# Performance work log

Measured on AMD Instinct MI355X. Metric: run time of the kernel, lower is better.

## Reference

```python
import jax, jax.numpy as jnp
import numpy as np

TEMPERATURE = 30.0
NUM_KERNELS = 4


def setup_inputs() -> dict:
    key = jax.random.key(0)
    ks = jax.random.split(key, 7)
    B, H, W, C = 32, 56, 56, 256
    F, KH, KW, K = 256, 3, 3, NUM_KERNELS
    hidden = C // 4  # attention_reduction_ratio = 4
    x = jax.random.normal(ks[0], (B, H, W, C), dtype=jnp.float32)
    # K parallel conv kernels (HWIO layout) and biases
    fan = KH * KW * C
    kernels = jax.random.normal(ks[1], (K, KH, KW, C, F), dtype=jnp.float32) / np.sqrt(fan)
    biases = jnp.zeros((K, F), dtype=jnp.float32)
    # attention MLP: GAP -> Dense(C//4, relu) -> Dense(K)
    w1 = jax.random.normal(ks[2], (C, hidden), dtype=jnp.float32) / np.sqrt(C)
    b1 = jnp.zeros((hidden,), dtype=jnp.float32)
    w2 = jax.random.normal(ks[3], (hidden, K), dtype=jnp.float32) / np.sqrt(hidden)
    b2 = jnp.zeros((K,), dtype=jnp.float32)
    return {"x": x, "kernels": kernels, "biases": biases,
            "w1": w1, "b1": b1, "w2": w2, "b2": b2}


def reference(x, kernels, biases, w1, b1, w2, b2):
    # Attention router: GAP -> Dense(relu) -> Dense(K) -> softmax(logits / tau)
    pooled = jnp.mean(x, axis=(1, 2))                       # [B, C]
    h = jax.nn.relu(pooled @ w1 + b1)                       # [B, C//4]
    logits = h @ w2 + b2                                    # [B, K]
    attn = jax.nn.softmax(logits / TEMPERATURE, axis=-1)    # [B, K]

    # K parallel conv branches (stride 1, SAME padding, dilation 1, groups 1)
    def conv_k(w, b):
        y = jax.lax.conv_general_dilated(
            x, w, window_strides=(1, 1), padding='SAME',
            dimension_numbers=('NHWC', 'HWIO', 'NHWC'))
        return y + b                                        # [B, H, W, F]

    ys = jax.vmap(conv_k)(kernels, biases)                  # [K, B, H, W, F]
    # per-sample weighted aggregation of branch outputs
    out = jnp.einsum('kbhwf,bk->bhwf', ys, attn)            # [B, H, W, F]
    return out
```

## Files before the change

kernel.cpp:

```cpp
#include <hip/hip_runtime.h>
#include <hip/hip_bf16.h>
#include <stdint.h>

typedef __bf16 bf16_t;
typedef __bf16 bf16x4 __attribute__((ext_vector_type(4)));
typedef __bf16 bf16x8 __attribute__((ext_vector_type(8)));
typedef float floatx4 __attribute__((ext_vector_type(4)));

#define B_ 32
#define HP 58
#define WP 66

#define XPAD_OFF   0u
#define WAGG_OFF   62717952u
#define POOLED_OFF 100466688u
#define ATTN_OFF   100499456u
#define BIASAGG_OFF 100499968u

__device__ __forceinline__ void async_copy16(const void* gsrc, void* ldst) {
  __builtin_amdgcn_global_load_lds(
      (const __attribute__((address_space(1))) unsigned int*)gsrc,
      (__attribute__((address_space(3))) unsigned int*)ldst, 16, 0, 0);
}

__global__ __launch_bounds__(256)
void pad_pool(const float* __restrict__ x, bf16_t* __restrict__ xpad,
              float* __restrict__ pooled) {
  const int hp = blockIdx.x;
  const int b  = blockIdx.y;
  const int t  = threadIdx.x;
  const int c4 = (t & 63) << 2;
  const int wq = t >> 6;
  const int h  = hp - 1;
  const bool hvalid = (h >= 0) && (h < 56);
  bf16_t* dst = xpad + ((size_t)(b * 58 + hp)) * (66 * 256);
  const float* srcrow = x + ((size_t)(b * 56 + (hvalid ? h : 0))) * (56 * 256);
  floatx4 sum = {0.f, 0.f, 0.f, 0.f};
  for (int wp = wq; wp < 66; wp += 4) {
    const int w = wp - 1;
    floatx4 v = {0.f, 0.f, 0.f, 0.f};
    if (hvalid && (unsigned)w < 56u) {
      v = *(const floatx4*)(srcrow + w * 256 + c4);
      sum += v;
    }
    bf16x4 r;
#pragma unroll
    for (int j = 0; j < 4; ++j) r[j] = (bf16_t)v[j];
    *(bf16x4*)(dst + wp * 256 + c4) = r;
  }
  __shared__ floatx4 red[4][64];
  red[wq][t & 63] = sum;
  __syncthreads();
  if (hvalid && t < 64) {
    floatx4 s = red[0][t] + red[1][t] + red[2][t] + red[3][t];
#pragma unroll
    for (int j = 0; j < 4; ++j) atomicAdd(&pooled[b * 256 + t * 4 + j], s[j]);
  }
}

__global__ __launch_bounds__(256)
void router(const float* __restrict__ pooled, const float* __restrict__ w1,
            const float* __restrict__ b1, const float* __restrict__ w2,
            const float* __restrict__ b2, const float* __restrict__ biases,
            float* __restrict__ attn, float* __restrict__ biasagg) {
  __shared__ float ps[8192];
  __shared__ float w1s[16384];
  __shared__ float hs[2048];
  __shared__ float lg[128];
  __shared__ float at[128];
  const int t = threadIdx.x;
  for (int i = t; i < 8192; i += 256) ps[i] = pooled[i] * (1.0f / 3136.0f);
  for (int i = t; i < 4096; i += 256)
    *(floatx4*)&w1s[i * 4] = *(const floatx4*)&w1[i * 4];
  __syncthreads();
  for (int task = t; task < 2048; task += 256) {
    const int b = task >> 6, j = task & 63;
    const float* pb = ps + b * 256;
    float s0 = 0.f, s1 = 0.f, s2 = 0.f, s3 = 0.f;
#pragma unroll 4
    for (int c = 0; c < 256; c += 4) {
      s0 += pb[c]     * w1s[c * 64 + j];
      s1 += pb[c + 1] * w1s[(c + 1) * 64 + j];
      s2 += pb[c + 2] * w1s[(c + 2) * 64 + j];
      s3 += pb[c + 3] * w1s[(c + 3) * 64 + j];
    }
    hs[task] = fmaxf((s0 + s1) + (s2 + s3) + b1[j], 0.f);
  }
  __syncthreads();
  if (t < 128) {
    int b = t >> 2, k = t & 3;
    float s = b2[k];
    const float* hb = hs + b * 64;
#pragma unroll 4
    for (int j = 0; j < 64; ++j) s += hb[j] * w2[j * 4 + k];
    lg[t] = s * (1.0f / 30.0f);
  }
  __syncthreads();
  if (t < 32) {
    int b = t;
    float z0 = lg[b*4], z1 = lg[b*4+1], z2 = lg[b*4+2], z3 = lg[b*4+3];
    float m = fmaxf(fmaxf(z0, z1), fmaxf(z2, z3));
    float e0 = expf(z0-m), e1 = expf(z1-m), e2 = expf(z2-m), e3 = expf(z3-m);
    float inv = 1.0f / (e0 + e1 + e2 + e3);
    at[b*4] = e0*inv; at[b*4+1] = e1*inv; at[b*4+2] = e2*inv; at[b*4+3] = e3*inv;
    attn[b*4] = at[b*4]; attn[b*4+1] = at[b*4+1];
    attn[b*4+2] = at[b*4+2]; attn[b*4+3] = at[b*4+3];
  }
  __syncthreads();
  for (int i = t; i < 8192; i += 256) {
    int b = i >> 8, f = i & 255;
    biasagg[i] = at[b*4]*biases[f] + at[b*4+1]*biases[256+f]
               + at[b*4+2]*biases[512+f] + at[b*4+3]*biases[768+f];
  }
}

__global__ __launch_bounds__(256)
void wagg_kernel(const float* __restrict__ kers, const float* __restrict__ attn,
                 bf16_t* __restrict__ wagg) {
  const int lid = blockIdx.x;
  const int xcd = lid & 7;
  const int sl  = lid >> 3;
  const int c8  = sl & 7;
  const int tap = sl >> 3;
  const int b0  = xcd << 2;
  const int t   = threadIdx.x;
  __shared__ bf16_t tile[4][32 * 260];

  float a[4][4];
#pragma unroll
  for (int i = 0; i < 4; ++i)
#pragma unroll
    for (int k = 0; k < 4; ++k) a[i][k] = attn[(b0 + i) * 4 + k];

  const float* k0 = kers + ((size_t)(0 * 9 + tap)) * 65536 + (size_t)(c8 * 32) * 256;
  const float* k1 = kers + ((size_t)(1 * 9 + tap)) * 65536 + (size_t)(c8 * 32) * 256;
  const float* k2 = kers + ((size_t)(2 * 9 + tap)) * 65536 + (size_t)(c8 * 32) * 256;
  const float* k3 = kers + ((size_t)(3 * 9 + tap)) * 65536 + (size_t)(c8 * 32) * 256;

  const int fq = t & 63;
  const int cl = t >> 6;
  const int f0 = fq * 4;
#pragma unroll
  for (int pass = 0; pass < 8; ++pass) {
    const int c_local = pass * 4 + cl;
    const size_t o = (size_t)c_local * 256 + f0;
    floatx4 v0 = *(const floatx4*)(k0 + o);
    floatx4 v1 = *(const floatx4*)(k1 + o);
    floatx4 v2 = *(const floatx4*)(k2 + o);
    floatx4 v3 = *(const floatx4*)(k3 + o);
#pragma unroll
    for (int i = 0; i < 4; ++i) {
      bf16x4 r;
#pragma unroll
      for (int j = 0; j < 4; ++j)
        r[j] = (bf16_t)(a[i][0] * v0[j] + a[i][1] * v1[j] + a[i][2] * v2[j] + a[i][3] * v3[j]);
      *(bf16x4*)&tile[i][c_local * 260 + f0] = r;
    }
  }
  __syncthreads();

#pragma unroll
  for (int i = 0; i < 4; ++i) {
    bf16_t* wt = wagg + ((size_t)((b0 + i) * 9 + tap)) * 65536 + c8 * 32;
#pragma unroll
    for (int pass = 0; pass < 4; ++pass) {
      const int gi = pass * 256 + t;
      const int f  = gi >> 2;
      const int cg = gi & 3;
      bf16x8 v;
#pragma unroll
      for (int jj = 0; jj < 8; ++jj) v[jj] = tile[i][(cg * 8 + jj) * 260 + f];
      *(bf16x8*)(wt + (size_t)f * 256 + cg * 8) = v;
    }
  }
}

#define PBUF_BYTES 40960

__global__ __launch_bounds__(512, 2)
void conv_mfma(const bf16_t* __restrict__ xpad, const bf16_t* __restrict__ wagg,
               const float* __restrict__ biasagg, float* __restrict__ out) {
  __shared__ char lds[2 * PBUF_BYTES];
  char* ldsP0 = lds;
  char* ldsP1 = lds + PBUF_BYTES;

  const int lid  = blockIdx.y * 14 + blockIdx.x;
  const int nid  = (lid & 7) * 56 + (lid >> 3);
  const int b    = nid / 14;
  const int tile = nid - b * 14;
  const int h0 = (tile >> 1) * 8;
  const int w0 = (tile & 1) * 28;

  const int tid  = threadIdx.x;
  const int lane = tid & 63;
  const int wv   = tid >> 6;
  const int mg   = wv >> 2;
  const int fs   = wv & 3;
  const int l15  = lane & 15;
  const int quad = lane >> 4;
  const int n0   = fs * 64;

  const char* xb = (const char*)xpad + (size_t)b * (HP * WP * 256 * 2);
  const char* wb = (const char*)wagg + (size_t)b * (9 * 256 * 256 * 2);

  int offs[7];
#pragma unroll
  for (int mi = 0; mi < 7; ++mi) {
    int m = mg * 112 + mi * 16 + l15;
    int ty = m / 28;
    int tx = m - ty * 28;
    offs[mi] = ty * 32 + tx;
  }
  const char* bbase = wb + (size_t)(n0 + l15) * 512 + quad * 16;
  int sp_off[5];
#pragma unroll
  for (int ii = 0; ii < 5; ++ii) {
    int i40 = wv * 5 + ii;
    int p = i40 * 8 + (lane >> 3);
    int row = p >> 5, col = p & 31;
    int gsrc = (lane & 7) ^ (p & 7);
    sp_off[ii] = ((h0 + row) * WP + (w0 + col)) * 512 + gsrc * 16;
  }

  floatx4 acc[7][4];
#pragma unroll
  for (int mi = 0; mi < 7; ++mi)
#pragma unroll
    for (int ni = 0; ni < 4; ++ni) acc[mi][ni] = (floatx4){0.f, 0.f, 0.f, 0.f};

  auto stage_patch = [&](int cq, char* pdst) {
#pragma unroll
    for (int ii = 0; ii < 5; ++ii)
      async_copy16(xb + cq * 128 + sp_off[ii], pdst + (wv * 5 + ii) * 1024);
  };
  auto load_B = [&](int cq, int tap, bf16x8* dst) {
    const char* base = bbase + (size_t)tap * 131072 + cq * 128;
#pragma unroll
    for (int ni = 0; ni < 4; ++ni) {
      dst[ni]     = *(const bf16x8*)(base + ni * 8192);
      dst[4 + ni] = *(const bf16x8*)(base + ni * 8192 + 64);
    }
  };

  stage_patch(0, ldsP0);
  asm volatile("s_waitcnt vmcnt(0)" ::: "memory");
  __builtin_amdgcn_s_barrier();
  __builtin_amdgcn_sched_barrier(0);

  bf16x8 Bcur[8], Bnext[8];
  load_B(0, 0, Bcur);

  bf16x8 aA[7], aB[7];

#pragma unroll 1
  for (int d = 0; d < 36; ++d) {
    const int cq  = d / 9;
    const int tap = d - cq * 9;
    char* pbc = (cq & 1) ? ldsP1 : ldsP0;
    char* pbn = (cq & 1) ? ldsP0 : ldsP1;
    const bool haveNext = (d < 35);

    if (tap == 0 && cq < 3) stage_patch(cq + 1, pbn);

    if (haveNext) {
      const int nt = (tap == 8) ? 0 : tap + 1;
      const int nc = (tap == 8) ? cq + 1 : cq;
      load_B(nc, nt, Bnext);
    }

    const int tapoff = (tap / 3) * 32 + (tap % 3);
    int aoff[7];
#pragma unroll
    for (int mi = 0; mi < 7; ++mi) {
      int p = offs[mi] + tapoff;
      aoff[mi] = (p << 7) + ((quad ^ (p & 7)) << 4);
      aA[mi] = *(const bf16x8*)(pbc + aoff[mi]);
    }

    __builtin_amdgcn_s_setprio(1);
#pragma unroll
    for (int mi = 0; mi < 7; ++mi) {
      acc[mi][0] = __builtin_amdgcn_mfma_f32_16x16x32_bf16(aA[mi], Bcur[0], acc[mi][0], 0, 0, 0);
      acc[mi][1] = __builtin_amdgcn_mfma_f32_16x16x32_bf16(aA[mi], Bcur[1], acc[mi][1], 0, 0, 0);
      acc[mi][2] = __builtin_amdgcn_mfma_f32_16x16x32_bf16(aA[mi], Bcur[2], acc[mi][2], 0, 0, 0);
      acc[mi][3] = __builtin_amdgcn_mfma_f32_16x16x32_bf16(aA[mi], Bcur[3], acc[mi][3], 0, 0, 0);
    }
    __builtin_amdgcn_s_setprio(0);

#pragma unroll
    for (int mi = 0; mi < 7; ++mi)
      aB[mi] = *(const bf16x8*)(pbc + (aoff[mi] ^ 64));

    __builtin_amdgcn_s_setprio(1);
#pragma unroll
    for (int mi = 0; mi < 7; ++mi) {
      acc[mi][0] = __builtin_amdgcn_mfma_f32_16x16x32_bf16(aB[mi], Bcur[4], acc[mi][0], 0, 0, 0);
      acc[mi][1] = __builtin_amdgcn_mfma_f32_16x16x32_bf16(aB[mi], Bcur[5], acc[mi][1], 0, 0, 0);
      acc[mi][2] = __builtin_amdgcn_mfma_f32_16x16x32_bf16(aB[mi], Bcur[6], acc[mi][2], 0, 0, 0);
      acc[mi][3] = __builtin_amdgcn_mfma_f32_16x16x32_bf16(aB[mi], Bcur[7], acc[mi][3], 0, 0, 0);
    }
    __builtin_amdgcn_s_setprio(0);

    if (tap == 8 && cq < 3) {
      asm volatile("s_waitcnt vmcnt(0)" ::: "memory");
      __builtin_amdgcn_s_barrier();
      __builtin_amdgcn_sched_barrier(0);
    }

    if (haveNext) {
#pragma unroll
      for (int i = 0; i < 8; ++i) Bcur[i] = Bnext[i];
    }
  }

  float bias[4];
#pragma unroll
  for (int ni = 0; ni < 4; ++ni) bias[ni] = biasagg[b * 256 + n0 + ni * 16 + l15];
  float* outb = out + (size_t)b * (56 * 56 * 256);
#pragma unroll
  for (int mi = 0; mi < 7; ++mi) {
#pragma unroll
    for (int rg = 0; rg < 4; ++rg) {
      int m = mg * 112 + mi * 16 + quad * 4 + rg;
      int ty = m / 28, tx = m - ty * 28;
      float* orow = outb + ((size_t)((h0 + ty) * 56) + (w0 + tx)) * 256 + n0 + l15;
#pragma unroll
      for (int ni = 0; ni < 4; ++ni) orow[ni * 16] = acc[mi][ni][rg] + bias[ni];
    }
  }
}

extern "C" void kernel_launch(void* const* d_in, const int* in_sizes, int n_in,
                              void* d_out, int out_size, void* d_ws, size_t ws_size,
                              hipStream_t stream) {
  const float* x      = (const float*)d_in[0];
  const float* kers   = (const float*)d_in[1];
  const float* biases = (const float*)d_in[2];
  const float* w1     = (const float*)d_in[3];
  const float* b1     = (const float*)d_in[4];
  const float* w2     = (const float*)d_in[5];
  const float* b2     = (const float*)d_in[6];
  float* outp = (float*)d_out;
  char* ws = (char*)d_ws;

  bf16_t* xpad   = (bf16_t*)(ws + XPAD_OFF);
  bf16_t* wagg   = (bf16_t*)(ws + WAGG_OFF);
  float* pooled  = (float*)(ws + POOLED_OFF);
  float* attn    = (float*)(ws + ATTN_OFF);
  float* biasagg = (float*)(ws + BIASAGG_OFF);

  hipMemsetAsync(pooled, 0, 32 * 256 * sizeof(float), stream);
  pad_pool<<<dim3(58, 32), 256, 0, stream>>>(x, xpad, pooled);
  router<<<1, 256, 0, stream>>>(pooled, w1, b1, w2, b2, biases, attn, biasagg);
  wagg_kernel<<<dim3(576), 256, 0, stream>>>(kers, attn, wagg);
  conv_mfma<<<dim3(14, 32), 512, 0, stream>>>(xpad, wagg, biasagg, outp);
}
```

Baseline: 401.8 us.

## Pre-swizzle aggregated weights into MFMA fragment order and ping-pong B registers

The weight-aggregation kernel now writes the per-sample bf16 weights in an order that matches the MFMA B-fragment layout, so each lane in the conv kernel reads contiguous 16-byte chunks at 1 KB strides. Previously each lane gathered from rows 512 bytes apart. The conv main loop is also unrolled by two, alternating between two B register sets instead of copying Bnext into Bcur every step. The goal is more coalesced global loads for B and fewer register moves, at the cost of a more complex write pattern in wagg_kernel and more code.

New measurement: 371.6 us. -7.5%, faster.

```diff
diff --git a/kernel.cpp b/kernel.cpp
--- a/kernel.cpp
+++ b/kernel.cpp
@@ -122,6 +122,8 @@
   const int sl  = lid >> 3;
   const int c8  = sl & 7;
   const int tap = sl >> 3;
+  const int cq  = c8 >> 1;
+  const int ks  = c8 & 1;
   const int b0  = xcd << 2;
   const int t   = threadIdx.x;
   __shared__ bf16_t tile[4][32 * 260];
@@ -161,16 +163,20 @@
 
 #pragma unroll
   for (int i = 0; i < 4; ++i) {
-    bf16_t* wt = wagg + ((size_t)((b0 + i) * 9 + tap)) * 65536 + c8 * 32;
+    char* wt = (char*)wagg + (size_t)(b0 + i) * 1179648 + (size_t)tap * 131072
+             + cq * 32768 + ks * 4096;
 #pragma unroll
     for (int pass = 0; pass < 4; ++pass) {
-      const int gi = pass * 256 + t;
-      const int f  = gi >> 2;
-      const int cg = gi & 3;
+      const int gi  = pass * 256 + t;
+      const int l15g = gi & 15;
+      const int q    = (gi >> 4) & 3;
+      const int ni   = (gi >> 6) & 3;
+      const int fs   = gi >> 8;
+      const int f    = fs * 64 + ni * 16 + l15g;
       bf16x8 v;
 #pragma unroll
-      for (int jj = 0; jj < 8; ++jj) v[jj] = tile[i][(cg * 8 + jj) * 260 + f];
-      *(bf16x8*)(wt + (size_t)f * 256 + cg * 8) = v;
+      for (int j = 0; j < 8; ++j) v[j] = tile[i][(q * 8 + j) * 260 + f];
+      *(bf16x8*)(wt + fs * 8192 + ni * 1024 + q * 256 + l15g * 16) = v;
     }
   }
 }
@@ -201,7 +207,7 @@
   const int n0   = fs * 64;
 
   const char* xb = (const char*)xpad + (size_t)b * (HP * WP * 256 * 2);
-  const char* wb = (const char*)wagg + (size_t)b * (9 * 256 * 256 * 2);
+  const char* wb = (const char*)wagg + (size_t)b * 1179648 + fs * 8192 + (size_t)lane * 16;
 
   int offs[7];
 #pragma unroll
@@ -211,7 +217,6 @@
     int tx = m - ty * 28;
     offs[mi] = ty * 32 + tx;
   }
-  const char* bbase = wb + (size_t)(n0 + l15) * 512 + quad * 16;
   int sp_off[5];
 #pragma unroll
   for (int ii = 0; ii < 5; ++ii) {
@@ -233,12 +238,65 @@
     for (int ii = 0; ii < 5; ++ii)
       async_copy16(xb + cq * 128 + sp_off[ii], pdst + (wv * 5 + ii) * 1024);
   };
-  auto load_B = [&](int cq, int tap, bf16x8* dst) {
-    const char* base = bbase + (size_t)tap * 131072 + cq * 128;
-#pragma unroll
-    for (int ni = 0; ni < 4; ++ni) {
-      dst[ni]     = *(const bf16x8*)(base + ni * 8192);
-      dst[4 + ni] = *(const bf16x8*)(base + ni * 8192 + 64);
+  auto load_B = [&](int cq, int tap, bf16x8 (&dst)[8]) {
+    const char* base = wb + (size_t)tap * 131072 + cq * 32768;
+#pragma unroll
+    for (int idx = 0; idx < 8; ++idx)
+      dst[idx] = *(const bf16x8*)(base + idx * 1024);
+  };
+
+  auto step = [&](int d, bf16x8 (&cur)[8], bf16x8 (&nxt)[8]) {
+    const int cq  = d / 9;
+    const int tap = d - cq * 9;
+    char* pbc = (cq & 1) ? ldsP1 : ldsP0;
+    char* pbn = (cq & 1) ? ldsP0 : ldsP1;
+
+    if (tap == 0 && cq < 3) stage_patch(cq + 1, pbn);
+
+    if (d < 35) {
+      const int nt = (tap == 8) ? 0 : tap + 1;
+      const int nc = (tap == 8) ? cq + 1 : cq;
+      load_B(nc, nt, nxt);
+    }
+
+    const int tapoff = (tap / 3) * 32 + (tap % 3);
+    int aoff[7];
+    bf16x8 aA[7], aB[7];
+#pragma unroll
+    for (int mi = 0; mi < 7; ++mi) {
+      int p = offs[mi] + tapoff;
+      aoff[mi] = (p << 7) + ((quad ^ (p & 7)) << 4);
+      aA[mi] = *(const bf16x8*)(pbc + aoff[mi]);
+    }
+
+    __builtin_amdgcn_s_setprio(1);
+#pragma unroll
+    for (int mi = 0; mi < 7; ++mi) {
+      acc[mi][0] = __builtin_amdgcn_mfma_f32_16x16x32_bf16(aA[mi], cur[0], acc[mi][0], 0, 0, 0);
+      acc[mi][1] = __builtin_amdgcn_mfma_f32_16x16x32_bf16(aA[mi], cur[1], acc[mi][1], 0, 0, 0);
+      acc[mi][2] = __builtin_amdgcn_mfma_f32_16x16x32_bf16(aA[mi], cur[2], acc[mi][2], 0, 0, 0);
+      acc[mi][3] = __builtin_amdgcn_mfma_f32_16x16x32_bf16(aA[mi], cur[3], acc[mi][3], 0, 0, 0);
+    }
+    __builtin_amdgcn_s_setprio(0);
+
+#pragma unroll
+    for (int mi = 0; mi < 7; ++mi)
+      aB[mi] = *(const bf16x8*)(pbc + (aoff[mi] ^ 64));
+
+    __builtin_amdgcn_s_setprio(1);
+#pragma unroll
+    for (int mi = 0; mi < 7; ++mi) {
+      acc[mi][0] = __builtin_amdgcn_mfma_f32_16x16x32_bf16(aB[mi], cur[4], acc[mi][0], 0, 0, 0);
+      acc[mi][1] = __builtin_amdgcn_mfma_f32_16x16x32_bf16(aB[mi], cur[5], acc[mi][1], 0, 0, 0);
+      acc[mi][2] = __builtin_amdgcn_mfma_f32_16x16x32_bf16(aB[mi], cur[6], acc[mi][2], 0, 0, 0);
+      acc[mi][3] = __builtin_amdgcn_mfma_f32_16x16x32_bf16(aB[mi], cur[7], acc[mi][3], 0, 0, 0);
+    }
+    __builtin_amdgcn_s_setprio(0);
+
+    if (tap == 8 && cq < 3) {
+      asm volatile("s_waitcnt vmcnt(0)" ::: "memory");
+      __builtin_amdgcn_s_barrier();
+      __builtin_amdgcn_sched_barrier(0);
     }
   };
 
@@ -247,70 +305,13 @@
   __builtin_amdgcn_s_barrier();
   __builtin_amdgcn_sched_barrier(0);
 
-  bf16x8 Bcur[8], Bnext[8];
-  load_B(0, 0, Bcur);
-
-  bf16x8 aA[7], aB[7];
+  bf16x8 BA[8], BB[8];
+  load_B(0, 0, BA);
 
 #pragma unroll 1
-  for (int d = 0; d < 36; ++d) {
-    const int cq  = d / 9;
-    const int tap = d - cq * 9;
-    char* pbc = (cq & 1) ? ldsP1 : ldsP0;
-    char* pbn = (cq & 1) ? ldsP0 : ldsP1;
-    const bool haveNext = (d < 35);
-
-    if (tap == 0 && cq < 3) stage_patch(cq + 1, pbn);
-
-    if (haveNext) {
-      const int nt = (tap == 8) ? 0 : tap + 1;
-      const int nc = (tap == 8) ? cq + 1 : cq;
-      load_B(nc, nt, Bnext);
-    }
-
-    const int tapoff = (tap / 3) * 32 + (tap % 3);
-    int aoff[7];
-#pragma unroll
-    for (int mi = 0; mi < 7; ++mi) {
-      int p = offs[mi] + tapoff;
-      aoff[mi] = (p << 7) + ((quad ^ (p & 7)) << 4);
-      aA[mi] = *(const bf16x8*)(pbc + aoff[mi]);
-    }
-
-    __builtin_amdgcn_s_setprio(1);
-#pragma unroll
-    for (int mi = 0; mi < 7; ++mi) {
-      acc[mi][0] = __builtin_amdgcn_mfma_f32_16x16x32_bf16(aA[mi], Bcur[0], acc[mi][0], 0, 0, 0);
-      acc[mi][1] = __builtin_amdgcn_mfma_f32_16x16x32_bf16(aA[mi], Bcur[1], acc[mi][1], 0, 0, 0);
-      acc[mi][2] = __builtin_amdgcn_mfma_f32_16x16x32_bf16(aA[mi], Bcur[2], acc[mi][2], 0, 0, 0);
-      acc[mi][3] = __builtin_amdgcn_mfma_f32_16x16x32_bf16(aA[mi], Bcur[3], acc[mi][3], 0, 0, 0);
-    }
-    __builtin_amdgcn_s_setprio(0);
-
-#pragma unroll
-    for (int mi = 0; mi < 7; ++mi)
-      aB[mi] = *(const bf16x8*)(pbc + (aoff[mi] ^ 64));
-
-    __builtin_amdgcn_s_setprio(1);
-#pragma unroll
-    for (int mi = 0; mi < 7; ++mi) {
-      acc[mi][0] = __builtin_amdgcn_mfma_f32_16x16x32_bf16(aB[mi], Bcur[4], acc[mi][0], 0, 0, 0);
-      acc[mi][1] = __builtin_amdgcn_mfma_f32_16x16x32_bf16(aB[mi], Bcur[5], acc[mi][1], 0, 0, 0);
-      acc[mi][2] = __builtin_amdgcn_mfma_f32_16x16x32_bf16(aB[mi], Bcur[6], acc[mi][2], 0, 0, 0);
-      acc[mi][3] = __builtin_amdgcn_mfma_f32_16x16x32_bf16(aB[mi], Bcur[7], acc[mi][3], 0, 0, 0);
-    }
-    __builtin_amdgcn_s_setprio(0);
-
-    if (tap == 8 && cq < 3) {
-      asm volatile("s_waitcnt vmcnt(0)" ::: "memory");
-      __builtin_amdgcn_s_barrier();
-      __builtin_amdgcn_sched_barrier(0);
-    }
-
-    if (haveNext) {
-#pragma unroll
-      for (int i = 0; i < 8; ++i) Bcur[i] = Bnext[i];
-    }
+  for (int dp = 0; dp < 18; ++dp) {
+    step(2 * dp,     BA, BB);
+    step(2 * dp + 1, BB, BA);
   }
 
   float bias[4];
```
